# Kernel tuning notes

Hardware: AMD Instinct MI355X
Metric: run time of the kernel (lower is better)

The kernel has to match this reference:

```python
import jax, jax.numpy as jnp
import numpy as np
from jax import lax

D_MODEL = 256
D_STATE = 16
BATCH = 4
SEQ = 16384
LN_EPS = 1e-5


def setup_inputs() -> dict:
    key = jax.random.key(0)
    ks = jax.random.split(key, 16)
    d, s = D_MODEL, D_STATE
    lim = 1.0 / np.sqrt(d)
    u = lambda k, shape, l: jax.random.uniform(k, shape, jnp.float32, -l, l)
    return {
        "x": jax.random.normal(ks[0], (BATCH, SEQ, d), jnp.float32),
        # forward branch params (torch Linear stored as (in, out))
        "W_fproj": u(ks[1], (d, 2 * d), lim),
        "b_fproj": u(ks[2], (2 * d,), lim),
        "A_f": jax.random.normal(ks[3], (s, d), jnp.float32),
        "W_fgate": u(ks[4], (d, s), lim),
        "b_fgate": u(ks[5], (s,), lim),
        # backward branch params
        "W_bproj": u(ks[6], (d, 2 * d), lim),
        "b_bproj": u(ks[7], (2 * d,), lim),
        "A_b": jax.random.normal(ks[8], (s, d), jnp.float32),
        "W_bgate": u(ks[9], (d, s), lim),
        "b_bgate": u(ks[10], (s,), lim),
        # output proj + layernorm
        "W_out": u(ks[11], (2 * d, d), 1.0 / np.sqrt(2 * d)),
        "b_out": u(ks[12], (d,), 1.0 / np.sqrt(2 * d)),
        "ln_g": jnp.ones((d,), jnp.float32),
        "ln_b": jnp.zeros((d,), jnp.float32),
    }


def _scan_dir(x, W_proj, b_proj, A, W_gate, b_gate):
    """One direction: gated state-space scan. x: (B,S,D) -> (B,S,D)."""
    B, S, D = x.shape
    proj = x @ W_proj + b_proj            # (B,S,2D)
    value = proj[..., D:]                 # the 'gate' chunk is unused in the original
    gw = jax.nn.sigmoid(value @ W_gate + b_gate)  # (B,S,d_state)

    def step(state, inp):
        g, v = inp                        # g:(B,Ns), v:(B,D)
        gi = g[:, :, None]                # (B,Ns,1)
        upd = A[None, :, :] * v[:, None, :]
        state = state * gi + upd * (1.0 - gi)
        out = (state * gi).sum(axis=1)    # (B,D)
        return state, out

    init = jnp.zeros((B, A.shape[0], D), x.dtype)
    _, outs = lax.scan(step, init, (gw.transpose(1, 0, 2), value.transpose(1, 0, 2)))
    return outs.transpose(1, 0, 2)        # (B,S,D)


def reference(x, W_fproj, b_fproj, A_f, W_fgate, b_fgate,
              W_bproj, b_bproj, A_b, W_bgate, b_bgate,
              W_out, b_out, ln_g, ln_b):
    fwd = _scan_dir(x, W_fproj, b_fproj, A_f, W_fgate, b_fgate)
    x_rev = jnp.flip(x, axis=1)
    bwd = jnp.flip(_scan_dir(x_rev, W_bproj, b_bproj, A_b, W_bgate, b_bgate), axis=1)
    combined = jnp.concatenate([fwd, bwd], axis=-1)    # (B,S,2D)
    out = combined @ W_out + b_out                     # (B,S,D)
    mu = out.mean(axis=-1, keepdims=True)
    var = out.var(axis=-1, keepdims=True)
    out = (out - mu) * lax.rsqrt(var + LN_EPS) * ln_g + ln_b
    return out  # dropout is identity in eval mode
```

## Files before the change

kernel.cpp:

```cpp
#include <hip/hip_runtime.h>

#define SEQ   16384
#define NB    4
#define NROWS 65536
#define NC    512
#define CL    32

typedef short bf16x8 __attribute__((ext_vector_type(8)));
typedef float f32x4  __attribute__((ext_vector_type(4)));
typedef float f32x2  __attribute__((ext_vector_type(2)));

__device__ inline float bf2f(ushort u) {
    unsigned int t = ((unsigned int)u) << 16;
    float f; __builtin_memcpy(&f, &t, 4); return f;
}
__device__ inline float bflo(uint u) {
    uint t = u << 16; float f; __builtin_memcpy(&f, &t, 4); return f;
}
__device__ inline float bfhi(uint u) {
    uint t = u & 0xffff0000u; float f; __builtin_memcpy(&f, &t, 4); return f;
}
__device__ inline ushort f2bf(float f) {
    unsigned int b; __builtin_memcpy(&b, &f, 4);
    unsigned int r = (b + 0x7FFFu + ((b >> 16) & 1u)) >> 16;
    return (ushort)r;
}
__device__ inline uint cvt_pk_bf16(float lo, float hi) {
    uint r;
    asm("v_cvt_pk_bf16_f32 %0, %1, %2" : "=v"(r) : "v"(lo), "v"(hi));
    return r;
}

__device__ inline f32x2 pk_fma(f32x2 a, f32x2 b, f32x2 c) {
    f32x2 d;
    asm("v_pk_fma_f32 %0, %1, %2, %3" : "=v"(d) : "v"(a), "v"(b), "v"(c));
    return d;
}
__device__ inline f32x2 pk_mul(f32x2 a, f32x2 b) {
    f32x2 d;
    asm("v_pk_mul_f32 %0, %1, %2" : "=v"(d) : "v"(a), "v"(b));
    return d;
}
__device__ inline f32x2 pk_sub(f32x2 a, f32x2 b) {
    f32x2 d;
    asm("v_pk_add_f32 %0, %1, %2 neg_lo:[0,1] neg_hi:[0,1]" : "=v"(d) : "v"(a), "v"(b));
    return d;
}

__global__ __launch_bounds__(256) void prep_weights(
    const float* __restrict__ Wf, const float* __restrict__ Wb,
    const float* __restrict__ Wo, const float* __restrict__ Wgf,
    const float* __restrict__ Wgb, const float* __restrict__ bfp,
    const float* __restrict__ bbp, const float* __restrict__ A_f,
    const float* __restrict__ A_b,
    ushort* __restrict__ BTv, ushort* __restrict__ WoT,
    ushort* __restrict__ WgT, float* __restrict__ bias_v,
    float* __restrict__ AsT)
{
    int idx = blockIdx.x * 256 + threadIdx.x;
    if (idx < 131072) {
        int dir = idx >> 16, j = idx & 65535, n = j >> 8, k = j & 255;
        const float* W = dir ? Wb : Wf;
        BTv[idx] = f2bf(W[k * 512 + 256 + n]);
    } else if (idx < 262144) {
        int j = idx - 131072; int n = j >> 9, k = j & 511;
        WoT[j] = f2bf(Wo[k * 256 + n]);
    } else if (idx < 270336) {
        int j = idx - 262144; int dir = j >> 12, jj = j & 4095, s = jj >> 8, k = jj & 255;
        WgT[j] = f2bf((dir ? Wgb : Wgf)[k * 16 + s]);
    } else if (idx < 270848) {
        int j = idx - 270336; int dir = j >> 8, n = j & 255;
        bias_v[j] = (dir ? bbp : bfp)[256 + n];
    } else if (idx < 279040) {
        int j = idx - 270848; int dir = j >> 12, jj = j & 4095, d = jj >> 4, s = jj & 15;
        AsT[j] = (dir ? A_b : A_f)[s * 256 + d];
    }
}

__global__ __launch_bounds__(512) void gemm_value(
    const float* __restrict__ x, const ushort* __restrict__ BTv,
    const float* __restrict__ bias_v, ushort* __restrict__ value)
{
    __shared__ ushort Al[128 * 40];
    __shared__ ushort Bl[256 * 40];
    const int tid = threadIdx.x;
    const int m0 = blockIdx.y * 128, dir = blockIdx.x;
    const ushort* BT = BTv + dir * 65536;
    const int w = tid >> 6, l = tid & 63;
    const int wr = w >> 2, wc = w & 3;
    const int l15 = l & 15, lk = (l >> 4) * 8;
    f32x4 acc[4][4] = {};

    for (int kk = 0; kk < 256; kk += 32) {
        {
            int r = tid >> 2, c = (tid & 3) * 8;
            const float* xp = x + (size_t)(m0 + r) * 256 + kk + c;
            float4 a = *(const float4*)xp;
            float4 b = *(const float4*)(xp + 4);
            ushort u[8];
            u[0] = f2bf(a.x); u[1] = f2bf(a.y); u[2] = f2bf(a.z); u[3] = f2bf(a.w);
            u[4] = f2bf(b.x); u[5] = f2bf(b.y); u[6] = f2bf(b.z); u[7] = f2bf(b.w);
            *(uint4*)&Al[r * 40 + c] = *(uint4*)u;
        }
        #pragma unroll
        for (int i = 0; i < 2; ++i) {
            int idx = tid + i * 512; int r = idx >> 2, c = idx & 3;
            *(uint4*)&Bl[r * 40 + c * 8] = *(const uint4*)(BT + (size_t)r * 256 + kk + c * 8);
        }
        __syncthreads();
        bf16x8 af[4], bfr[4];
        #pragma unroll
        for (int m = 0; m < 4; ++m) af[m] = *(const bf16x8*)&Al[(wr * 64 + m * 16 + l15) * 40 + lk];
        #pragma unroll
        for (int n = 0; n < 4; ++n) bfr[n] = *(const bf16x8*)&Bl[(wc * 64 + n * 16 + l15) * 40 + lk];
        #pragma unroll
        for (int m = 0; m < 4; ++m)
            #pragma unroll
            for (int n = 0; n < 4; ++n)
                acc[m][n] = __builtin_amdgcn_mfma_f32_16x16x32_bf16(af[m], bfr[n], acc[m][n], 0, 0, 0);
        __syncthreads();
    }
    const int rbase = (l >> 4) * 4;
    #pragma unroll
    for (int m = 0; m < 4; ++m)
        #pragma unroll
        for (int n = 0; n < 4; ++n) {
            int col = wc * 64 + n * 16 + l15;
            float bv = bias_v[dir * 256 + col];
            #pragma unroll
            for (int r = 0; r < 4; ++r) {
                int row = m0 + wr * 64 + m * 16 + rbase + r;
                value[(size_t)row * 512 + dir * 256 + col] = f2bf(acc[m][n][r] + bv);
            }
        }
}

__global__ __launch_bounds__(512, 4) void gate_scan(
    ushort* __restrict__ value, const ushort* __restrict__ WgT,
    const float* __restrict__ bgf, const float* __restrict__ bgb,
    float* __restrict__ qg, ushort* __restrict__ L16, float* __restrict__ P,
    const float* __restrict__ AsT)
{
    __shared__ ushort Av[64 * 264];
    __shared__ float gsm[64 * 16];
    const int tid = threadIdx.x;
    const int r0 = blockIdx.x * 64, dir = blockIdx.y;
    #pragma unroll
    for (int i = 0; i < 4; ++i) {
        int idx = tid + i * 512; int r = idx >> 5, c = idx & 31;
        *(uint4*)&Av[r * 264 + c * 8] =
            *(const uint4*)(value + (size_t)(r0 + r) * 512 + dir * 256 + c * 8);
    }
    __syncthreads();
    const int w = tid >> 6, l = tid & 63, l15 = l & 15, lk = (l >> 4) * 8;
    const int b = r0 >> 14, t0 = r0 & 16383;
    if (w < 4) {
        const ushort* Wg = WgT + dir * 4096;
        f32x4 acc = {};
        #pragma unroll
        for (int kk = 0; kk < 256; kk += 32) {
            bf16x8 af = *(const bf16x8*)&Av[(w * 16 + l15) * 264 + kk + lk];
            bf16x8 bf = *(const bf16x8*)(Wg + l15 * 256 + kk + lk);
            acc = __builtin_amdgcn_mfma_f32_16x16x32_bf16(af, bf, acc, 0, 0, 0);
        }
        const float bgs = (dir ? bgb : bgf)[l15];
        const int rbase = (l >> 4) * 4;
        #pragma unroll
        for (int r = 0; r < 4; ++r) {
            int lr = w * 16 + rbase + r;
            float sv = 1.f / (1.f + __expf(-(acc[r] + bgs)));
            gsm[lr * 16 + l15] = sv;
        }
    }
    __syncthreads();
    if (tid < 32) {
        int ci = tid >> 4, s = tid & 15;
        float pfx = 1.f;
        float* qb = qg + ((size_t)(dir * NB + b) * SEQ + t0 + ci * 32) * 16 + s;
        for (int i = 0; i < CL; ++i) {
            int r = dir ? (CL - 1 - i) : i;
            float g = gsm[(ci * 32 + r) * 16 + s];
            pfx *= g;
            qb[r * 16] = g * pfx;
        }
        P[((size_t)(dir * NB + b) * NC + (t0 >> 5) + ci) * 16 + s] = pfx;
    }
    const int ci = tid >> 8, d = tid & 255;
    const int chunk = (t0 >> 5) + ci;
    const float* Ad = AsT + dir * 4096 + d * 16;
    f32x2 a[8], c[8] = {};
    #pragma unroll
    for (int sp = 0; sp < 8; ++sp) a[sp] = *(const f32x2*)(Ad + sp * 2);
    for (int i = 0; i < CL; ++i) {
        int row = dir ? (CL - 1 - i) : i;
        float v = bf2f(Av[(ci * 32 + row) * 264 + d]);
        f32x2 vd = {v, v};
        f32x2 o = {0.f, 0.f};
        const float* gr = &gsm[(ci * 32 + row) * 16];
        #pragma unroll
        for (int q4 = 0; q4 < 4; ++q4) {
            f32x4 G = *(const f32x4*)(gr + q4 * 4);
            f32x2 ga; ga.x = G.x; ga.y = G.y;
            f32x2 gb; gb.x = G.z; gb.y = G.w;
            int sa = q4 * 2, sb = q4 * 2 + 1;
            c[sa] = pk_fma(ga, pk_sub(c[sa], vd), vd);
            o = pk_fma(a[sa], pk_mul(ga, c[sa]), o);
            c[sb] = pk_fma(gb, pk_sub(c[sb], vd), vd);
            o = pk_fma(a[sb], pk_mul(gb, c[sb]), o);
        }
        Av[(ci * 32 + row) * 264 + d] = (ushort)cvt_pk_bf16(o.x + o.y, 0.f);
    }
    {
        uint ub[8];
        #pragma unroll
        for (int sp = 0; sp < 8; ++sp) ub[sp] = cvt_pk_bf16(c[sp].x, c[sp].y);
        ushort* Lp = L16 + ((size_t)(dir * NB + b) * NC + chunk) * 4096 + d * 16;
        *(uint4*)Lp       = *(uint4*)&ub[0];
        *(uint4*)(Lp + 8) = *(uint4*)&ub[4];
    }
    __syncthreads();
    #pragma unroll
    for (int i = 0; i < 4; ++i) {
        int idx = tid + i * 512; int r = idx >> 5, c = idx & 31;
        *(uint4*)(value + (size_t)(r0 + r) * 512 + dir * 256 + c * 8) =
            *(uint4*)&Av[r * 264 + c * 8];
    }
}

__global__ __launch_bounds__(256, 2) void chunk_scan(
    ushort* __restrict__ L16, const float* __restrict__ P)
{
    const int bid = blockIdx.x;
    const int dir = bid >> 6, b = (bid >> 4) & 3, dgrp = bid & 15;
    const int tid = threadIdx.x;
    const int s = tid & 15;
    const size_t cb = (size_t)(dir * NB + b) * NC;
    ushort* Lb = L16 + cb * 4096 + dgrp * 256 + tid;
    const float* Pb = P + cb * 16 + s;
    float e = 0.f;
    ushort lA[16], lB[16];
    float pA[16], pB[16];

#define LOADB(la, pa, ib) { _Pragma("unroll") \
    for (int j = 0; j < 16; ++j) { \
        int t = (ib) * 16 + j; int k = dir ? (NC - 1 - t) : t; \
        la[j] = Lb[(size_t)k * 4096]; pa[j] = Pb[k * 16]; } }
#define PROCB(la, pa, ib) { _Pragma("unroll") \
    for (int j = 0; j < 16; ++j) { \
        int t = (ib) * 16 + j; int k = dir ? (NC - 1 - t) : t; \
        Lb[(size_t)k * 4096] = f2bf(e); e = pa[j] * e + bf2f(la[j]); } }

    LOADB(lA, pA, 0)
    for (int ib = 0; ib < 32; ib += 2) {
        LOADB(lB, pB, ib + 1)
        PROCB(lA, pA, ib)
        if (ib + 2 < 32) { LOADB(lA, pA, ib + 2) }
        PROCB(lB, pB, ib + 1)
    }
#undef LOADB
#undef PROCB
}

__global__ __launch_bounds__(256) void pass_c(
    ushort* __restrict__ value, const float* __restrict__ qg,
    const ushort* __restrict__ L16, const float* __restrict__ AsT)
{
    const int chunk = blockIdx.x, b = blockIdx.y, dir = blockIdx.z;
    const int tid = threadIdx.x;
    __shared__ float qs[CL * 16];
    __shared__ ushort vs[CL * 256];
    const float* qd = qg + ((size_t)(dir * NB + b) * SEQ + chunk * CL) * 16;
    if (tid < 128) ((float4*)qs)[tid] = ((const float4*)qd)[tid];
    ushort* vg = value + ((size_t)b * SEQ + chunk * CL) * 512 + dir * 256;
    #pragma unroll
    for (int i = 0; i < 4; ++i) {
        int idx = tid + i * 256;
        int r = idx >> 5, cc = idx & 31;
        *(uint4*)&vs[r * 256 + cc * 8] = *(const uint4*)(vg + (size_t)r * 512 + cc * 8);
    }
    const int d = tid;
    const float* Ad = AsT + dir * 4096 + d * 16;
    const ushort* Lp = L16 + ((size_t)(dir * NB + b) * NC + chunk) * 4096 + d * 16;
    f32x2 h[8];
    #pragma unroll
    for (int sp = 0; sp < 8; ++sp) {
        f32x2 a = *(const f32x2*)(Ad + sp * 2);
        uint u = *(const uint*)(Lp + sp * 2);
        f32x2 E; E.x = bflo(u); E.y = bfhi(u);
        h[sp] = pk_mul(a, E);
    }
    __syncthreads();
    for (int row = 0; row < CL; ++row) {
        f32x2 corr = {0.f, 0.f};
        #pragma unroll
        for (int sp = 0; sp < 8; ++sp) {
            f32x2 q = *(const f32x2*)&qs[row * 16 + sp * 2];
            corr = pk_fma(q, h[sp], corr);
        }
        float outv = bf2f(vs[row * 256 + d]) + corr.x + corr.y;
        vs[row * 256 + d] = f2bf(outv);
    }
    __syncthreads();
    #pragma unroll
    for (int i = 0; i < 4; ++i) {
        int idx = tid + i * 256;
        int r = idx >> 5, cc = idx & 31;
        *(uint4*)(vg + (size_t)r * 512 + cc * 8) = *(uint4*)&vs[r * 256 + cc * 8];
    }
}

__global__ __launch_bounds__(512) void gemm_out_ln(
    const ushort* __restrict__ A, const ushort* __restrict__ BT,
    const float* __restrict__ b_out, const float* __restrict__ ln_g,
    const float* __restrict__ ln_b, float* __restrict__ out)
{
    __shared__ ushort Al[128 * 40];
    __shared__ ushort Bl[256 * 40];
    __shared__ float red[2][2][4][64];
    const int tid = threadIdx.x;
    const int m0 = blockIdx.x * 128;
    const int w = tid >> 6, l = tid & 63;
    const int wr = w >> 2, wc = w & 3;
    const int l15 = l & 15, lk = (l >> 4) * 8;
    f32x4 acc[4][4] = {};

    for (int kk = 0; kk < 512; kk += 32) {
        {
            int r = tid >> 2, c = tid & 3;
            *(uint4*)&Al[r * 40 + c * 8] = *(const uint4*)(A + (size_t)(m0 + r) * 512 + kk + c * 8);
        }
        #pragma unroll
        for (int i = 0; i < 2; ++i) {
            int idx = tid + i * 512; int r = idx >> 2, c = idx & 3;
            *(uint4*)&Bl[r * 40 + c * 8] = *(const uint4*)(BT + (size_t)r * 512 + kk + c * 8);
        }
        __syncthreads();
        bf16x8 af[4], bfr[4];
        #pragma unroll
        for (int m = 0; m < 4; ++m) af[m] = *(const bf16x8*)&Al[(wr * 64 + m * 16 + l15) * 40 + lk];
        #pragma unroll
        for (int n = 0; n < 4; ++n) bfr[n] = *(const bf16x8*)&Bl[(wc * 64 + n * 16 + l15) * 40 + lk];
        #pragma unroll
        for (int m = 0; m < 4; ++m)
            #pragma unroll
            for (int n = 0; n < 4; ++n)
                acc[m][n] = __builtin_amdgcn_mfma_f32_16x16x32_bf16(af[m], bfr[n], acc[m][n], 0, 0, 0);
        __syncthreads();
    }
    const int rbase = (l >> 4) * 4;
    float gg[4], bb[4];
    #pragma unroll
    for (int n = 0; n < 4; ++n) {
        int col = wc * 64 + n * 16 + l15;
        float bv = b_out[col];
        gg[n] = ln_g[col]; bb[n] = ln_b[col];
        #pragma unroll
        for (int m = 0; m < 4; ++m)
            #pragma unroll
            for (int r = 0; r < 4; ++r)
                acc[m][n][r] += bv;
    }
    float s1[4][4], s2[4][4];
    #pragma unroll
    for (int m = 0; m < 4; ++m)
        #pragma unroll
        for (int r = 0; r < 4; ++r) {
            float a_ = 0.f, b_ = 0.f;
            #pragma unroll
            for (int n = 0; n < 4; ++n) {
                float v = acc[m][n][r];
                a_ += v; b_ += v * v;
            }
            s1[m][r] = a_; s2[m][r] = b_;
        }
    #pragma unroll
    for (int mask = 1; mask < 16; mask <<= 1)
        #pragma unroll
        for (int m = 0; m < 4; ++m)
            #pragma unroll
            for (int r = 0; r < 4; ++r) {
                s1[m][r] += __shfl_xor(s1[m][r], mask, 64);
                s2[m][r] += __shfl_xor(s2[m][r], mask, 64);
            }
    if (l15 == 0) {
        #pragma unroll
        for (int m = 0; m < 4; ++m)
            #pragma unroll
            for (int r = 0; r < 4; ++r) {
                int row = m * 16 + rbase + r;
                red[0][wr][wc][row] = s1[m][r];
                red[1][wr][wc][row] = s2[m][r];
            }
    }
    __syncthreads();
    #pragma unroll
    for (int m = 0; m < 4; ++m)
        #pragma unroll
        for (int r = 0; r < 4; ++r) {
            int row = m * 16 + rbase + r;
            float t1 = red[0][wr][0][row] + red[0][wr][1][row] + red[0][wr][2][row] + red[0][wr][3][row];
            float t2 = red[1][wr][0][row] + red[1][wr][1][row] + red[1][wr][2][row] + red[1][wr][3][row];
            float mu = t1 * (1.f / 256.f);
            float var = t2 * (1.f / 256.f) - mu * mu;
            float rs = rsqrtf(var + 1e-5f);
            #pragma unroll
            for (int n = 0; n < 4; ++n) {
                int col = wc * 64 + n * 16 + l15;
                out[(size_t)(m0 + wr * 64 + row) * 256 + col] = (acc[m][n][r] - mu) * rs * gg[n] + bb[n];
            }
        }
}

extern "C" void kernel_launch(void* const* d_in, const int* in_sizes, int n_in,
                              void* d_out, int out_size, void* d_ws, size_t ws_size,
                              hipStream_t stream)
{
    const float* x       = (const float*)d_in[0];
    const float* W_fproj = (const float*)d_in[1];
    const float* b_fproj = (const float*)d_in[2];
    const float* A_f     = (const float*)d_in[3];
    const float* W_fgate = (const float*)d_in[4];
    const float* b_fgate = (const float*)d_in[5];
    const float* W_bproj = (const float*)d_in[6];
    const float* b_bproj = (const float*)d_in[7];
    const float* A_b     = (const float*)d_in[8];
    const float* W_bgate = (const float*)d_in[9];
    const float* b_bgate = (const float*)d_in[10];
    const float* W_out   = (const float*)d_in[11];
    const float* b_out   = (const float*)d_in[12];
    const float* ln_g    = (const float*)d_in[13];
    const float* ln_b    = (const float*)d_in[14];

    char* ws = (char*)d_ws;
    ushort* value  = (ushort*)(ws + 0);
    float*  qg     = (float*) (ws + 67108864);
    ushort* L16    = (ushort*)(ws + 75497472);
    float*  P      = (float*) (ws + 109051904);
    ushort* BTv    = (ushort*)(ws + 109314048);
    ushort* WoT    = (ushort*)(ws + 109576192);
    ushort* WgT    = (ushort*)(ws + 109838336);
    float*  bias_v = (float*) (ws + 109854720);
    float*  AsT    = (float*) (ws + 109856768);

    prep_weights<<<1090, 256, 0, stream>>>(W_fproj, W_bproj, W_out, W_fgate, W_bgate,
                                           b_fproj, b_bproj, A_f, A_b,
                                           BTv, WoT, WgT, bias_v, AsT);
    gemm_value<<<dim3(2, 512), 512, 0, stream>>>(x, BTv, bias_v, value);
    gate_scan<<<dim3(1024, 2), 512, 0, stream>>>(value, WgT, b_fgate, b_bgate, qg, L16, P, AsT);
    chunk_scan<<<128, 256, 0, stream>>>(L16, P);
    pass_c<<<dim3(NC, NB, 2), 256, 0, stream>>>(value, qg, L16, AsT);
    gemm_out_ln<<<512, 512, 0, stream>>>(value, WoT, b_out, ln_g, ln_b, (float*)d_out);
}
```

Measured before the change: 213.2 us.

## Fold gate projection into value GEMM via precomposed weights, split scan kernel

Precomputes W_value·W_gate and the folded gate bias in prep_weights, so the gate logits come straight from x inside gemm_value as an extra MFMA column block, with the sigmoid written to a new gw buffer. The old gate_scan kernel's gate GEMM is removed and a lighter scan_kernel (one 32-row chunk per 256-thread block) reads gw. This drops the dependent gate GEMM on value and restructures the scan launch, at the cost of an extra fp32 gw write and read. The prep kernel also gains a serial 256-length dot product per element, and the composed weights are rounded to bf16, which changes numerics slightly.

```diff
diff --git a/kernel.cpp b/kernel.cpp
--- a/kernel.cpp
+++ b/kernel.cpp
@@ -51,11 +51,12 @@
     const float* __restrict__ Wf, const float* __restrict__ Wb,
     const float* __restrict__ Wo, const float* __restrict__ Wgf,
     const float* __restrict__ Wgb, const float* __restrict__ bfp,
-    const float* __restrict__ bbp, const float* __restrict__ A_f,
+    const float* __restrict__ bbp, const float* __restrict__ bgf,
+    const float* __restrict__ bgb, const float* __restrict__ A_f,
     const float* __restrict__ A_b,
     ushort* __restrict__ BTv, ushort* __restrict__ WoT,
-    ushort* __restrict__ WgT, float* __restrict__ bias_v,
-    float* __restrict__ AsT)
+    ushort* __restrict__ BTg, float* __restrict__ bias_v,
+    float* __restrict__ AsT, float* __restrict__ bvg)
 {
     int idx = blockIdx.x * 256 + threadIdx.x;
     if (idx < 131072) {
@@ -67,22 +68,38 @@
         WoT[j] = f2bf(Wo[k * 256 + n]);
     } else if (idx < 270336) {
         int j = idx - 262144; int dir = j >> 12, jj = j & 4095, s = jj >> 8, k = jj & 255;
-        WgT[j] = f2bf((dir ? Wgb : Wgf)[k * 16 + s]);
+        const float* Wv = (dir ? Wb : Wf) + k * 512 + 256;
+        const float* Wg = dir ? Wgb : Wgf;
+        float acc = 0.f;
+        #pragma unroll 8
+        for (int n = 0; n < 256; ++n) acc += Wv[n] * Wg[n * 16 + s];
+        BTg[j] = f2bf(acc);
     } else if (idx < 270848) {
         int j = idx - 270336; int dir = j >> 8, n = j & 255;
         bias_v[j] = (dir ? bbp : bfp)[256 + n];
     } else if (idx < 279040) {
         int j = idx - 270848; int dir = j >> 12, jj = j & 4095, d = jj >> 4, s = jj & 15;
         AsT[j] = (dir ? A_b : A_f)[s * 256 + d];
+    } else if (idx < 279072) {
+        int j = idx - 279040; int dir = j >> 4, s = j & 15;
+        const float* bp = (dir ? bbp : bfp) + 256;
+        const float* Wg = dir ? Wgb : Wgf;
+        float acc = (dir ? bgb : bgf)[s];
+        #pragma unroll 8
+        for (int n = 0; n < 256; ++n) acc += bp[n] * Wg[n * 16 + s];
+        bvg[j] = acc;
     }
 }
 
 __global__ __launch_bounds__(512) void gemm_value(
     const float* __restrict__ x, const ushort* __restrict__ BTv,
-    const float* __restrict__ bias_v, ushort* __restrict__ value)
+    const ushort* __restrict__ BTg, const float* __restrict__ bias_v,
+    const float* __restrict__ bvg, ushort* __restrict__ value,
+    float* __restrict__ gw)
 {
     __shared__ ushort Al[128 * 40];
     __shared__ ushort Bl[256 * 40];
+    __shared__ ushort Bgl[16 * 40];
     const int tid = threadIdx.x;
     const int m0 = blockIdx.y * 128, dir = blockIdx.x;
     const ushort* BT = BTv + dir * 65536;
@@ -90,6 +107,7 @@
     const int wr = w >> 2, wc = w & 3;
     const int l15 = l & 15, lk = (l >> 4) * 8;
     f32x4 acc[4][4] = {};
+    f32x4 accg[4] = {};
 
     for (int kk = 0; kk < 256; kk += 32) {
         {
@@ -107,6 +125,10 @@
             int idx = tid + i * 512; int r = idx >> 2, c = idx & 3;
             *(uint4*)&Bl[r * 40 + c * 8] = *(const uint4*)(BT + (size_t)r * 256 + kk + c * 8);
         }
+        if (tid < 64) {
+            int r = tid >> 2, c = tid & 3;
+            *(uint4*)&Bgl[r * 40 + c * 8] = *(const uint4*)(BTg + dir * 4096 + r * 256 + kk + c * 8);
+        }
         __syncthreads();
         bf16x8 af[4], bfr[4];
         #pragma unroll
@@ -118,6 +140,12 @@
             #pragma unroll
             for (int n = 0; n < 4; ++n)
                 acc[m][n] = __builtin_amdgcn_mfma_f32_16x16x32_bf16(af[m], bfr[n], acc[m][n], 0, 0, 0);
+        if (wc == 0) {
+            bf16x8 bg_ = *(const bf16x8*)&Bgl[l15 * 40 + lk];
+            #pragma unroll
+            for (int m = 0; m < 4; ++m)
+                accg[m] = __builtin_amdgcn_mfma_f32_16x16x32_bf16(af[m], bg_, accg[m], 0, 0, 0);
+        }
         __syncthreads();
     }
     const int rbase = (l >> 4) * 4;
@@ -133,70 +161,49 @@
                 value[(size_t)row * 512 + dir * 256 + col] = f2bf(acc[m][n][r] + bv);
             }
         }
-}
-
-__global__ __launch_bounds__(512, 4) void gate_scan(
-    ushort* __restrict__ value, const ushort* __restrict__ WgT,
-    const float* __restrict__ bgf, const float* __restrict__ bgb,
+    if (wc == 0) {
+        float bgs = bvg[dir * 16 + l15];
+        #pragma unroll
+        for (int m = 0; m < 4; ++m)
+            #pragma unroll
+            for (int r = 0; r < 4; ++r) {
+                int gr = m0 + wr * 64 + m * 16 + rbase + r;
+                int bb_ = gr >> 14, tt = gr & 16383;
+                float sv = 1.f / (1.f + __expf(-(accg[m][r] + bgs)));
+                gw[((size_t)(dir * NB + bb_) * SEQ + tt) * 16 + l15] = sv;
+            }
+    }
+}
+
+__global__ __launch_bounds__(256) void scan_kernel(
+    ushort* __restrict__ value, const float* __restrict__ gw,
     float* __restrict__ qg, ushort* __restrict__ L16, float* __restrict__ P,
     const float* __restrict__ AsT)
 {
-    __shared__ ushort Av[64 * 264];
-    __shared__ float gsm[64 * 16];
+    const int chunk = blockIdx.x, b = blockIdx.y, dir = blockIdx.z;
     const int tid = threadIdx.x;
-    const int r0 = blockIdx.x * 64, dir = blockIdx.y;
+    __shared__ float gs[CL * 16];
+    __shared__ ushort Av[CL * 264];
+    const float* gwd = gw + ((size_t)(dir * NB + b) * SEQ + chunk * CL) * 16;
+    if (tid < 128) ((float4*)gs)[tid] = ((const float4*)gwd)[tid];
+    ushort* vg = value + ((size_t)b * SEQ + chunk * CL) * 512 + dir * 256;
     #pragma unroll
     for (int i = 0; i < 4; ++i) {
-        int idx = tid + i * 512; int r = idx >> 5, c = idx & 31;
-        *(uint4*)&Av[r * 264 + c * 8] =
-            *(const uint4*)(value + (size_t)(r0 + r) * 512 + dir * 256 + c * 8);
+        int idx = tid + i * 256; int r = idx >> 5, c = idx & 31;
+        *(uint4*)&Av[r * 264 + c * 8] = *(const uint4*)(vg + (size_t)r * 512 + c * 8);
     }
     __syncthreads();
-    const int w = tid >> 6, l = tid & 63, l15 = l & 15, lk = (l >> 4) * 8;
-    const int b = r0 >> 14, t0 = r0 & 16383;
-    if (w < 4) {
-        const ushort* Wg = WgT + dir * 4096;
-        f32x4 acc = {};
-        #pragma unroll
-        for (int kk = 0; kk < 256; kk += 32) {
-            bf16x8 af = *(const bf16x8*)&Av[(w * 16 + l15) * 264 + kk + lk];
-            bf16x8 bf = *(const bf16x8*)(Wg + l15 * 256 + kk + lk);
-            acc = __builtin_amdgcn_mfma_f32_16x16x32_bf16(af, bf, acc, 0, 0, 0);
-        }
-        const float bgs = (dir ? bgb : bgf)[l15];
-        const int rbase = (l >> 4) * 4;
-        #pragma unroll
-        for (int r = 0; r < 4; ++r) {
-            int lr = w * 16 + rbase + r;
-            float sv = 1.f / (1.f + __expf(-(acc[r] + bgs)));
-            gsm[lr * 16 + l15] = sv;
-        }
-    }
-    __syncthreads();
-    if (tid < 32) {
-        int ci = tid >> 4, s = tid & 15;
-        float pfx = 1.f;
-        float* qb = qg + ((size_t)(dir * NB + b) * SEQ + t0 + ci * 32) * 16 + s;
-        for (int i = 0; i < CL; ++i) {
-            int r = dir ? (CL - 1 - i) : i;
-            float g = gsm[(ci * 32 + r) * 16 + s];
-            pfx *= g;
-            qb[r * 16] = g * pfx;
-        }
-        P[((size_t)(dir * NB + b) * NC + (t0 >> 5) + ci) * 16 + s] = pfx;
-    }
-    const int ci = tid >> 8, d = tid & 255;
-    const int chunk = (t0 >> 5) + ci;
+    const int d = tid;
     const float* Ad = AsT + dir * 4096 + d * 16;
     f32x2 a[8], c[8] = {};
     #pragma unroll
     for (int sp = 0; sp < 8; ++sp) a[sp] = *(const f32x2*)(Ad + sp * 2);
     for (int i = 0; i < CL; ++i) {
         int row = dir ? (CL - 1 - i) : i;
-        float v = bf2f(Av[(ci * 32 + row) * 264 + d]);
+        float v = bf2f(Av[row * 264 + d]);
         f32x2 vd = {v, v};
         f32x2 o = {0.f, 0.f};
-        const float* gr = &gsm[(ci * 32 + row) * 16];
+        const float* gr = &gs[row * 16];
         #pragma unroll
         for (int q4 = 0; q4 < 4; ++q4) {
             f32x4 G = *(const f32x4*)(gr + q4 * 4);
@@ -208,7 +215,7 @@
             c[sb] = pk_fma(gb, pk_sub(c[sb], vd), vd);
             o = pk_fma(a[sb], pk_mul(gb, c[sb]), o);
         }
-        Av[(ci * 32 + row) * 264 + d] = (ushort)cvt_pk_bf16(o.x + o.y, 0.f);
+        Av[row * 264 + d] = (ushort)cvt_pk_bf16(o.x + o.y, 0.f);
     }
     {
         uint ub[8];
@@ -218,12 +225,23 @@
         *(uint4*)Lp       = *(uint4*)&ub[0];
         *(uint4*)(Lp + 8) = *(uint4*)&ub[4];
     }
+    if (tid < 16) {
+        const int s = tid;
+        float pfx = 1.f;
+        float* qb = qg + ((size_t)(dir * NB + b) * SEQ + chunk * CL) * 16 + s;
+        for (int i = 0; i < CL; ++i) {
+            int r = dir ? (CL - 1 - i) : i;
+            float g = gs[r * 16 + s];
+            pfx *= g;
+            qb[r * 16] = g * pfx;
+        }
+        P[((size_t)(dir * NB + b) * NC + chunk) * 16 + s] = pfx;
+    }
     __syncthreads();
     #pragma unroll
     for (int i = 0; i < 4; ++i) {
-        int idx = tid + i * 512; int r = idx >> 5, c = idx & 31;
-        *(uint4*)(value + (size_t)(r0 + r) * 512 + dir * 256 + c * 8) =
-            *(uint4*)&Av[r * 264 + c * 8];
+        int idx = tid + i * 256; int r = idx >> 5, c = idx & 31;
+        *(uint4*)(vg + (size_t)r * 512 + c * 8) = *(uint4*)&Av[r * 264 + c * 8];
     }
 }
 
@@ -433,20 +451,22 @@
 
     char* ws = (char*)d_ws;
     ushort* value  = (ushort*)(ws + 0);
-    float*  qg     = (float*) (ws + 67108864);
-    ushort* L16    = (ushort*)(ws + 75497472);
-    float*  P      = (float*) (ws + 109051904);
-    ushort* BTv    = (ushort*)(ws + 109314048);
-    ushort* WoT    = (ushort*)(ws + 109576192);
-    ushort* WgT    = (ushort*)(ws + 109838336);
-    float*  bias_v = (float*) (ws + 109854720);
-    float*  AsT    = (float*) (ws + 109856768);
-
-    prep_weights<<<1090, 256, 0, stream>>>(W_fproj, W_bproj, W_out, W_fgate, W_bgate,
-                                           b_fproj, b_bproj, A_f, A_b,
-                                           BTv, WoT, WgT, bias_v, AsT);
-    gemm_value<<<dim3(2, 512), 512, 0, stream>>>(x, BTv, bias_v, value);
-    gate_scan<<<dim3(1024, 2), 512, 0, stream>>>(value, WgT, b_fgate, b_bgate, qg, L16, P, AsT);
+    float*  gw     = (float*) (ws + 67108864);
+    float*  qg     = (float*) (ws + 75497472);
+    ushort* L16    = (ushort*)(ws + 83886080);
+    float*  P      = (float*) (ws + 117440512);
+    ushort* BTv    = (ushort*)(ws + 117702656);
+    ushort* WoT    = (ushort*)(ws + 117964800);
+    ushort* BTg    = (ushort*)(ws + 118226944);
+    float*  bias_v = (float*) (ws + 118243328);
+    float*  AsT    = (float*) (ws + 118245376);
+    float*  bvg    = (float*) (ws + 118278144);
+
+    prep_weights<<<1091, 256, 0, stream>>>(W_fproj, W_bproj, W_out, W_fgate, W_bgate,
+                                           b_fproj, b_bproj, b_fgate, b_bgate, A_f, A_b,
+                                           BTv, WoT, BTg, bias_v, AsT, bvg);
+    gemm_value<<<dim3(2, 512), 512, 0, stream>>>(x, BTv, BTg, bias_v, bvg, value, gw);
+    scan_kernel<<<dim3(NC, NB, 2), 256, 0, stream>>>(value, gw, qg, L16, P, AsT);
     chunk_scan<<<128, 256, 0, stream>>>(L16, P);
     pass_c<<<dim3(NC, NB, 2), 256, 0, stream>>>(value, qg, L16, AsT);
     gemm_out_ln<<<512, 512, 0, stream>>>(value, WoT, b_out, ln_g, ln_b, (float*)d_out);
```

After: 240.2 us. 12.7% more time.
